# Optimization experiments

Measured on AMD Instinct MI355X. Metric: run time of the kernel, lower is better.

## Reference

```python
import jax, jax.numpy as jnp
import numpy as np

# ---- MPDM social-force hyperparameters (the `param` object in the torch code) ----
N = 4096            # number of agents (agent 0 = robot)
PED_SPEED = 1.5     # param.pedestrians_speed (max / desired speed, m/s)
ROBOT_SPEED = 1.5   # param.robot_speed
K = 2.0             # param.k   (goal-attraction relaxation gain)
ALPHA = 10.0        # param.alpha (repulsive force amplitude)
PED_RADIUS = 0.3    # param.ped_radius
PED_MASS = 60.0     # param.ped_mass
BETTA = 0.71        # param.betta (repulsive range)
DT = 0.4            # param.DT
A_COST = 4.0        # param.a (progress weight)
B_COST = 1.2        # param.b (blame range)
E_COST = 0.001      # param.e (numerical epsilon)
EPS = 1e-8


def setup_inputs() -> dict:
    key = jax.random.key(0)
    k1, k2, k3, k4 = jax.random.split(key, 4)
    pos = jax.random.normal(k1, (N, 2), dtype=jnp.float32) * 10.0   # spread agents over ~20x20 m
    vel = jax.random.normal(k2, (N, 2), dtype=jnp.float32) * 0.5
    state = jnp.concatenate([pos, vel], axis=1)                     # [N,4] = (x, y, vx, vy)
    goals = jax.random.normal(k3, (N, 2), dtype=jnp.float32) * 10.0
    cost = jnp.zeros((N, 1), dtype=jnp.float32)
    stacked = state                                                 # trajectory stack seed
    robot_init_pose = jax.random.normal(k4, (2,), dtype=jnp.float32) * 10.0
    return {"state": state, "cost": cost,
            "stacked_trajectories_for_visualizer": stacked,
            "goals": goals, "robot_init_pose": robot_init_pose}


def calc_forces(state, goals):
    pos = state[:, 0:2]
    vel = state[:, 2:4]
    # --- attractive force: relax toward desired velocity pointing at goal ---
    to_goal = goals - pos                                   # [N,2]
    dist_goal = jnp.linalg.norm(to_goal, axis=1, keepdims=True)
    e_goal = to_goal / (dist_goal + EPS)
    desired_speed = jnp.full((N, 1), PED_SPEED, dtype=state.dtype).at[0, 0].set(ROBOT_SPEED)
    attr_force = K * (desired_speed * e_goal - vel) * PED_MASS      # [N,2]
    # --- repulsive force: all-pairs exponential social force ---
    diff = pos[:, None, :] - pos[None, :, :]                # [N,N,2]
    d = jnp.sqrt(jnp.sum(diff * diff, axis=-1) + EPS)       # [N,N]
    n_ij = diff / d[..., None]                              # unit vectors
    mag = ALPHA * jnp.exp((2.0 * PED_RADIUS - d) / BETTA)   # [N,N]
    mag = mag * (1.0 - jnp.eye(N, dtype=state.dtype))       # no self-force
    rep_force = jnp.sum(mag[..., None] * n_ij, axis=1)      # [N,2]
    return rep_force, attr_force


def pose_propagation(F, state):
    pos = state[:, 0:2]
    vel = state[:, 2:4]
    vel_new = vel + (F / PED_MASS) * DT
    speed = jnp.linalg.norm(vel_new, axis=1, keepdims=True)
    # clamp speed to max pedestrian speed
    vel_new = vel_new * jnp.minimum(1.0, PED_SPEED / (speed + EPS))
    pos_new = pos + vel_new * DT
    return jnp.concatenate([pos_new, vel_new], axis=1)      # [N,4]


def calc_cost_function(goals, robot_init_pose, state_out):
    pos = state_out[:, 0:2]
    robot_pose = pos[0]
    # robot progress toward its goal (projection onto initial goal direction)
    goal_dir = goals[0] - robot_init_pose
    PG = jnp.dot(goal_dir, robot_pose - robot_init_pose) / (jnp.linalg.norm(goal_dir) + E_COST)
    # blame: pedestrians close to the robot
    dist_to_robot = jnp.sqrt(jnp.sum((pos - robot_pose) ** 2, axis=1) + E_COST)
    blame = jnp.exp(-dist_to_robot / B_COST)
    blame = blame.at[0].set(0.0)                            # robot does not blame itself
    return -A_COST * PG + blame                             # [N]


def reference(state, cost, stacked_trajectories_for_visualizer, goals, robot_init_pose):
    rf, af = calc_forces(state, goals)
    F = rf + af
    out = pose_propagation(F, state)
    temp = calc_cost_function(goals, robot_init_pose, out)
    new_cost = cost + temp.reshape(-1, 1)
    stacked = jnp.concatenate([stacked_trajectories_for_visualizer, state], axis=0)
    return (out, new_cost, stacked)
```

## Files before the change

kernel.cpp:

```cpp
#include <hip/hip_runtime.h>

#define NN 4096
#define CHUNK 128

__global__ __launch_bounds__(256) void rep_forces(const float* __restrict__ state,
                                                  float* __restrict__ rep) {
    __shared__ float2 sp[CHUNK];
    const int i = blockIdx.x * 256 + threadIdx.x;
    const int jbase = blockIdx.y * CHUNK;
    if (threadIdx.x < CHUNK) {
        float4 s = reinterpret_cast<const float4*>(state)[jbase + threadIdx.x];
        sp[threadIdx.x] = make_float2(s.x, s.y);
    }
    __syncthreads();

    const float4 me = reinterpret_cast<const float4*>(state)[i];
    const float px = me.x, py = me.y;
    float fx = 0.f, fy = 0.f;

    const float C1 = 1.40845070422535f;
    const float C0 = 3.14765551813f;

#pragma unroll 8
    for (int t = 0; t < CHUNK; ++t) {
        float2 q = sp[t];
        float dx = px - q.x;
        float dy = py - q.y;
        float d2 = fmaf(dx, dx, 1e-8f);
        d2 = fmaf(dy, dy, d2);
        float inv_d = rsqrtf(d2);
        float d = d2 * inv_d;
        float e = __expf(fmaf(-C1, d, C0));
        float w = e * inv_d;
        fx = fmaf(w, dx, fx);
        fy = fmaf(w, dy, fy);
    }
    atomicAdd(&rep[2 * i],     fx);
    atomicAdd(&rep[2 * i + 1], fy);
}

__global__ __launch_bounds__(256) void propagate(const float* __restrict__ state,
                                                 const float* __restrict__ goals,
                                                 const float* __restrict__ rep,
                                                 float* __restrict__ out_state,
                                                 float* __restrict__ stacked_second) {
    const int i = blockIdx.x * 256 + threadIdx.x;
    const float4 me = reinterpret_cast<const float4*>(state)[i];
    const float2 g  = reinterpret_cast<const float2*>(goals)[i];

    float tgx = g.x - me.x, tgy = g.y - me.y;
    float dist = sqrtf(tgx * tgx + tgy * tgy);
    float inv = 1.f / (dist + 1e-8f);
    float Fx = rep[2 * i]     + 180.f * (tgx * inv) - 120.f * me.z;
    float Fy = rep[2 * i + 1] + 180.f * (tgy * inv) - 120.f * me.w;

    float vnx = me.z + Fx * (0.4f / 60.f);
    float vny = me.w + Fy * (0.4f / 60.f);
    float speed = sqrtf(vnx * vnx + vny * vny);
    float scale = fminf(1.f, 1.5f / (speed + 1e-8f));
    vnx *= scale;
    vny *= scale;
    float pnx = me.x + vnx * 0.4f;
    float pny = me.y + vny * 0.4f;

    reinterpret_cast<float4*>(out_state)[i]      = make_float4(pnx, pny, vnx, vny);
    reinterpret_cast<float4*>(stacked_second)[i] = me;
}

__global__ __launch_bounds__(256) void cost_and_copy(const float* __restrict__ out_state,
                                                     const float* __restrict__ cost_in,
                                                     const float* __restrict__ goals,
                                                     const float* __restrict__ robot_init,
                                                     const float* __restrict__ stacked_in,
                                                     float* __restrict__ cost_out,
                                                     float* __restrict__ stacked_first) {
    const int i = blockIdx.x * 256 + threadIdx.x;

    float rx = out_state[0], ry = out_state[1];
    float r0x = robot_init[0], r0y = robot_init[1];
    float gdx = goals[0] - r0x, gdy = goals[1] - r0y;
    float PG = (gdx * (rx - r0x) + gdy * (ry - r0y))
             / (sqrtf(gdx * gdx + gdy * gdy) + 0.001f);

    float px = out_state[4 * i], py = out_state[4 * i + 1];
    float ddx = px - rx, ddy = py - ry;
    float dist = sqrtf(ddx * ddx + ddy * ddy + 0.001f);
    float blame = (i == 0) ? 0.f : __expf(-dist * (1.f / 1.2f));

    cost_out[i] = cost_in[i] + (-4.f * PG + blame);
    reinterpret_cast<float4*>(stacked_first)[i] =
        reinterpret_cast<const float4*>(stacked_in)[i];
}

extern "C" void kernel_launch(void* const* d_in, const int* in_sizes, int n_in,
                              void* d_out, int out_size, void* d_ws, size_t ws_size,
                              hipStream_t stream) {
    const float* state      = (const float*)d_in[0];
    const float* cost       = (const float*)d_in[1];
    const float* stacked_in = (const float*)d_in[2];
    const float* goals      = (const float*)d_in[3];
    const float* robot_init = (const float*)d_in[4];

    float* out          = (float*)d_out;
    float* out_state    = out;
    float* out_cost     = out + NN * 4;
    float* out_stacked  = out + NN * 5;

    float* rep = (float*)d_ws;

    hipMemsetAsync(rep, 0, NN * 2 * sizeof(float), stream);

    dim3 gridA(NN / 256, NN / CHUNK);
    rep_forces<<<gridA, 256, 0, stream>>>(state, rep);

    propagate<<<NN / 256, 256, 0, stream>>>(state, goals, rep,
                                            out_state, out_stacked + NN * 4);

    cost_and_copy<<<NN / 256, 256, 0, stream>>>(out_state, cost, goals, robot_init,
                                                stacked_in, out_cost, out_stacked);
}
```

Baseline: 76.57 us.

## Replace atomic force accumulation with per-chunk partial sums and raw exp2/rsq intrinsics

The pairwise repulsion kernel now writes one partial force per (agent, j-chunk) to workspace instead of doing atomicAdd. The propagate kernel sums those 64 partials itself, so the memset launch goes away. The chunk size is halved to 64 for more blocks. The exp and rsqrt calls become the raw amdgcn exp2/rsq builtins with the constants pre-scaled by log2(e). In exchange, propagate must read 2 MB of partials serially per thread, and the raw intrinsics skip range and denormal handling.

```diff
diff --git a/kernel.cpp b/kernel.cpp
--- a/kernel.cpp
+++ b/kernel.cpp
@@ -1,10 +1,11 @@
 #include <hip/hip_runtime.h>
 
 #define NN 4096
-#define CHUNK 128
+#define CHUNK 64
+#define NCHUNK (NN / CHUNK)
 
-__global__ __launch_bounds__(256) void rep_forces(const float* __restrict__ state,
-                                                  float* __restrict__ rep) {
+__global__ __launch_bounds__(256) void rep_partial(const float* __restrict__ state,
+                                                   float2* __restrict__ part) {
     __shared__ float2 sp[CHUNK];
     const int i = blockIdx.x * 256 + threadIdx.x;
     const int jbase = blockIdx.y * CHUNK;
@@ -18,41 +19,49 @@
     const float px = me.x, py = me.y;
     float fx = 0.f, fy = 0.f;
 
-    const float C1 = 1.40845070422535f;
-    const float C0 = 3.14765551813f;
+    const float C1E = 2.0319648462f;
+    const float C0E = 4.5411071f;
 
-#pragma unroll 8
+#pragma unroll 16
     for (int t = 0; t < CHUNK; ++t) {
         float2 q = sp[t];
         float dx = px - q.x;
         float dy = py - q.y;
         float d2 = fmaf(dx, dx, 1e-8f);
         d2 = fmaf(dy, dy, d2);
-        float inv_d = rsqrtf(d2);
+        float inv_d = __builtin_amdgcn_rsqf(d2);
         float d = d2 * inv_d;
-        float e = __expf(fmaf(-C1, d, C0));
+        float e = __builtin_amdgcn_exp2f(fmaf(-C1E, d, C0E));
         float w = e * inv_d;
         fx = fmaf(w, dx, fx);
         fy = fmaf(w, dy, fy);
     }
-    atomicAdd(&rep[2 * i],     fx);
-    atomicAdd(&rep[2 * i + 1], fy);
+    part[blockIdx.y * NN + i] = make_float2(fx, fy);
 }
 
 __global__ __launch_bounds__(256) void propagate(const float* __restrict__ state,
                                                  const float* __restrict__ goals,
-                                                 const float* __restrict__ rep,
+                                                 const float2* __restrict__ part,
                                                  float* __restrict__ out_state,
                                                  float* __restrict__ stacked_second) {
     const int i = blockIdx.x * 256 + threadIdx.x;
+
+    float Fx = 0.f, Fy = 0.f;
+#pragma unroll
+    for (int c = 0; c < NCHUNK; ++c) {
+        float2 p = part[c * NN + i];
+        Fx += p.x;
+        Fy += p.y;
+    }
+
     const float4 me = reinterpret_cast<const float4*>(state)[i];
     const float2 g  = reinterpret_cast<const float2*>(goals)[i];
 
     float tgx = g.x - me.x, tgy = g.y - me.y;
     float dist = sqrtf(tgx * tgx + tgy * tgy);
     float inv = 1.f / (dist + 1e-8f);
-    float Fx = rep[2 * i]     + 180.f * (tgx * inv) - 120.f * me.z;
-    float Fy = rep[2 * i + 1] + 180.f * (tgy * inv) - 120.f * me.w;
+    Fx += 180.f * (tgx * inv) - 120.f * me.z;
+    Fy += 180.f * (tgy * inv) - 120.f * me.w;
 
     float vnx = me.z + Fx * (0.4f / 60.f);
     float vny = me.w + Fy * (0.4f / 60.f);
@@ -85,7 +94,8 @@
     float px = out_state[4 * i], py = out_state[4 * i + 1];
     float ddx = px - rx, ddy = py - ry;
     float dist = sqrtf(ddx * ddx + ddy * ddy + 0.001f);
-    float blame = (i == 0) ? 0.f : __expf(-dist * (1.f / 1.2f));
+    float blame = (i == 0) ? 0.f
+                : __builtin_amdgcn_exp2f(dist * -1.2022458675f);
 
     cost_out[i] = cost_in[i] + (-4.f * PG + blame);
     reinterpret_cast<float4*>(stacked_first)[i] =
@@ -106,14 +116,12 @@
     float* out_cost     = out + NN * 4;
     float* out_stacked  = out + NN * 5;
 
-    float* rep = (float*)d_ws;
+    float2* part = (float2*)d_ws;
 
-    hipMemsetAsync(rep, 0, NN * 2 * sizeof(float), stream);
+    dim3 gridA(NN / 256, NCHUNK);
+    rep_partial<<<gridA, 256, 0, stream>>>(state, part);
 
-    dim3 gridA(NN / 256, NN / CHUNK);
-    rep_forces<<<gridA, 256, 0, stream>>>(state, rep);
-
-    propagate<<<NN / 256, 256, 0, stream>>>(state, goals, rep,
+    propagate<<<NN / 256, 256, 0, stream>>>(state, goals, part,
                                             out_state, out_stacked + NN * 4);
 
     cost_and_copy<<<NN / 256, 256, 0, stream>>>(out_state, cost, goals, robot_init,
```

Measured after the change: 72.38 us. 5.5% less time.
